# Optimization experiments

Hardware: AMD Instinct MI355X
Metric: run time of the kernel (lower is better)

The kernel has to match this reference:

```python
import jax, jax.numpy as jnp
import numpy as np
from jax.ops import segment_sum

N_NODES = 100000
N_EDGES = 1250000
IN_CH = 64
HID_CH = 64
OUT_CH = 32
NUM_GRAPHS = 128


def setup_inputs() -> dict:
    key = jax.random.key(0)
    ks = jax.random.split(key, 6)
    x = jax.random.normal(ks[0], (N_NODES, IN_CH), dtype=jnp.float32)
    edge_index = jax.random.randint(ks[1], (2, N_EDGES), 0, N_NODES, dtype=jnp.int64)
    batch = jnp.sort(jax.random.randint(ks[2], (N_NODES,), 0, NUM_GRAPHS, dtype=jnp.int64))
    # Glorot-ish scaled weights, zero biases (PyG GCNConv defaults)
    W1 = jax.random.normal(ks[3], (IN_CH, HID_CH), dtype=jnp.float32) * (1.0 / np.sqrt(IN_CH))
    b1 = jnp.zeros((HID_CH,), dtype=jnp.float32)
    W2 = jax.random.normal(ks[4], (HID_CH, OUT_CH), dtype=jnp.float32) * (1.0 / np.sqrt(HID_CH))
    b2 = jnp.zeros((OUT_CH,), dtype=jnp.float32)
    return {"x": x, "edge_index": edge_index, "batch": batch,
            "W1": W1, "b1": b1, "W2": W2, "b2": b2}


def _gcn_conv(x, W, b, src, dst, deg_inv_sqrt):
    # GCNConv: out = D^{-1/2} (A + I) D^{-1/2} (x W) + b
    h = x @ W  # [N, C_out]
    # per-edge normalized messages: gather -> scale -> scatter-add
    msgs = h[src] * (deg_inv_sqrt[src] * deg_inv_sqrt[dst])[:, None]  # [E, C_out]
    agg = segment_sum(msgs, dst, num_segments=N_NODES)
    # self-loop contribution: dinv[i]^2 * h[i]
    agg = agg + h * (deg_inv_sqrt * deg_inv_sqrt)[:, None]
    return agg + b


def reference(x, edge_index, batch, W1, b1, W2, b2):
    src, dst = edge_index[0], edge_index[1]
    # degree with self-loops (GCNConv add_self_loops=True, in-degree of dst)
    ones = jnp.ones((N_EDGES,), dtype=x.dtype)
    deg = segment_sum(ones, dst, num_segments=N_NODES) + 1.0
    deg_inv_sqrt = jax.lax.rsqrt(deg)

    h = _gcn_conv(x, W1, b1, src, dst, deg_inv_sqrt)
    h = jax.nn.relu(h)
    # dropout: eval mode -> identity
    h = _gcn_conv(h, W2, b2, src, dst, deg_inv_sqrt)

    # global mean pool over graphs in the batch
    sums = segment_sum(h, batch, num_segments=NUM_GRAPHS)  # [G, OUT_CH]
    counts = segment_sum(jnp.ones((N_NODES,), dtype=h.dtype), batch, num_segments=NUM_GRAPHS)
    return sums / jnp.maximum(counts, 1.0)[:, None]
```

## Files before the change

kernel.cpp:

```cpp
#include <hip/hip_runtime.h>

#define NN 100000
#define NE 1250000
#define CIN 64
#define CH 64
#define CO 32
#define NG 128
#define NBUCK 98
#define BSHIFT 10
#define EPB 2048
#define NBLKP ((NE + EPB - 1) / EPB)
#define PSLOT 16384
#define CSLOT 24576
#define NTILE (NN / 16)
#define GB ((NTILE + 3) / 4)

typedef unsigned short ushortT;
typedef __attribute__((ext_vector_type(8))) short bfrag;
typedef __attribute__((ext_vector_type(4))) float ffrag;

static __device__ inline ushortT f2bf(float v) {
  unsigned int u = __float_as_uint(v);
  u += 0x7FFFu + ((u >> 16) & 1u);
  return (ushortT)(u >> 16);
}
static __device__ inline float bf2f(ushortT s) {
  return __uint_as_float(((unsigned int)s) << 16);
}
static __device__ inline bfrag pack8(float4 lo, float4 hi) {
  bfrag r;
  r[0] = (short)f2bf(lo.x); r[1] = (short)f2bf(lo.y);
  r[2] = (short)f2bf(lo.z); r[3] = (short)f2bf(lo.w);
  r[4] = (short)f2bf(hi.x); r[5] = (short)f2bf(hi.y);
  r[6] = (short)f2bf(hi.z); r[7] = (short)f2bf(hi.w);
  return r;
}

static __global__ void k_zero(float* __restrict__ sums, int* __restrict__ bcursor,
                              const int* __restrict__ batch, float* __restrict__ counts,
                              const float* __restrict__ W1, ushortT* __restrict__ W1T,
                              const float* __restrict__ W2, ushortT* __restrict__ W2T,
                              ushortT* __restrict__ h) {
  int i = blockIdx.x * 256 + threadIdx.x;
  if (i < NG * CO) sums[i] = 0.0f;
  if (i < 128) bcursor[i] = i * PSLOT;
  if (i < CH) h[(size_t)NN * CH + i] = 0;
  if (i < CIN * CH) W1T[i] = f2bf(W1[(i & 63) * CH + (i >> 6)]);
  if (i < CH * CO) W2T[i] = f2bf(W2[(i & 63) * CO + (i >> 6)]);
  if (blockIdx.x == 0 && threadIdx.x < NG) {
    int g = threadIdx.x;
    int lo = 0, hi = NN;
    while (lo < hi) { int m = (lo + hi) >> 1; if (batch[m] < g) lo = m + 1; else hi = m; }
    int lb = lo;
    lo = 0; hi = NN;
    while (lo < hi) { int m = (lo + hi) >> 1; if (batch[m] <= g) lo = m + 1; else hi = m; }
    counts[g] = (float)(lo - lb);
  }
}

static __global__ __launch_bounds__(256) void k_part(const int* __restrict__ src,
                                                     const int* __restrict__ dst,
                                                     int* __restrict__ bcursor,
                                                     unsigned int* __restrict__ pairs) {
  __shared__ int lh[128], lbase[128], loff[128];
  if (threadIdx.x < 128) { lh[threadIdx.x] = 0; loff[threadIdx.x] = 0; }
  __syncthreads();
  int e0 = blockIdx.x * EPB, e1 = min(e0 + EPB, NE);
  for (int e = e0 + threadIdx.x; e < e1; e += 256)
    atomicAdd(&lh[dst[e] >> BSHIFT], 1);
  __syncthreads();
  if (threadIdx.x < 128) {
    int v = lh[threadIdx.x];
    lbase[threadIdx.x] = v ? atomicAdd(&bcursor[threadIdx.x], v) : 0;
  }
  __syncthreads();
  for (int e = e0 + threadIdx.x; e < e1; e += 256) {
    int d = dst[e], b = d >> BSHIFT;
    int o = atomicAdd(&loff[b], 1);
    pairs[lbase[b] + o] = (unsigned int)src[e] | ((unsigned int)(d & 1023) << 17);
  }
}

static __global__ __launch_bounds__(1024) void k_bucket(const unsigned int* __restrict__ pairs,
                                                        const int* __restrict__ bcursor,
                                                        int* __restrict__ rowstart,
                                                        int* __restrict__ degi,
                                                        float* __restrict__ dinv,
                                                        int* __restrict__ csr_src) {
  __shared__ int lh[1024];
  __shared__ int tmp[1024];
  __shared__ int cur[1024];
  int t = threadIdx.x;
  int b = blockIdx.x, nb = b << BSHIFT;
  lh[t] = 0;
  __syncthreads();
  int p0 = b * PSLOT, p1 = bcursor[b];
  for (int p = p0 + t; p < p1; p += 1024)
    atomicAdd(&lh[pairs[p] >> 17], 1);
  __syncthreads();
  int node = nb + t;
  int raw = lh[t];
  int pd = (raw + 7) & ~7;
  tmp[t] = pd;
  __syncthreads();
  for (int off = 1; off < 1024; off <<= 1) {
    int add = (t >= off) ? tmp[t - off] : 0;
    __syncthreads();
    tmp[t] += add;
    __syncthreads();
  }
  int ex = tmp[t] - pd;
  int rs = b * CSLOT + ex;
  if (node < NN) {
    rowstart[node] = rs;
    degi[node] = pd >> 3;
    dinv[node] = rsqrtf((float)raw + 1.0f);
  }
  cur[t] = rs;
  __syncthreads();
  for (int p = p0 + t; p < p1; p += 1024) {
    unsigned int pk = pairs[p];
    int pos = atomicAdd(&cur[pk >> 17], 1);
    csr_src[pos] = (int)(pk & 0x1FFFFu);
  }
  __syncthreads();
  for (int q = raw; q < pd; ++q) csr_src[rs + q] = NN;
}

static __global__ __launch_bounds__(256) void k_gemm1(const float* __restrict__ x,
                                                      const ushortT* __restrict__ W1T,
                                                      const float* __restrict__ dinv,
                                                      ushortT* __restrict__ h) {
  int wave = threadIdx.x >> 6, lane = threadIdx.x & 63;
  int tile = blockIdx.x * 4 + wave;
  if (tile >= NTILE) return;
  int m = lane & 15;
  int kb = (lane >> 4) * 8;
  int row = tile * 16 + m;
  const float* xr = x + (size_t)row * CIN;
  float4 a0l = *(const float4*)(xr + kb);
  float4 a0h = *(const float4*)(xr + kb + 4);
  float4 a1l = *(const float4*)(xr + kb + 32);
  float4 a1h = *(const float4*)(xr + kb + 36);
  bfrag A0 = pack8(a0l, a0h);
  bfrag A1 = pack8(a1l, a1h);
  int nl = lane & 15;
  ffrag z = {0.f, 0.f, 0.f, 0.f};
  bfrag B00 = *(const bfrag*)(W1T + (0 * 16 + nl) * CIN + kb);
  bfrag B01 = *(const bfrag*)(W1T + (0 * 16 + nl) * CIN + kb + 32);
  bfrag B10 = *(const bfrag*)(W1T + (1 * 16 + nl) * CIN + kb);
  bfrag B11 = *(const bfrag*)(W1T + (1 * 16 + nl) * CIN + kb + 32);
  bfrag B20 = *(const bfrag*)(W1T + (2 * 16 + nl) * CIN + kb);
  bfrag B21 = *(const bfrag*)(W1T + (2 * 16 + nl) * CIN + kb + 32);
  bfrag B30 = *(const bfrag*)(W1T + (3 * 16 + nl) * CIN + kb);
  bfrag B31 = *(const bfrag*)(W1T + (3 * 16 + nl) * CIN + kb + 32);
  ffrag c0 = __builtin_amdgcn_mfma_f32_16x16x32_bf16(A0, B00, z, 0, 0, 0);
  c0 = __builtin_amdgcn_mfma_f32_16x16x32_bf16(A1, B01, c0, 0, 0, 0);
  ffrag c1 = __builtin_amdgcn_mfma_f32_16x16x32_bf16(A0, B10, z, 0, 0, 0);
  c1 = __builtin_amdgcn_mfma_f32_16x16x32_bf16(A1, B11, c1, 0, 0, 0);
  ffrag c2 = __builtin_amdgcn_mfma_f32_16x16x32_bf16(A0, B20, z, 0, 0, 0);
  c2 = __builtin_amdgcn_mfma_f32_16x16x32_bf16(A1, B21, c2, 0, 0, 0);
  ffrag c3 = __builtin_amdgcn_mfma_f32_16x16x32_bf16(A0, B30, z, 0, 0, 0);
  c3 = __builtin_amdgcn_mfma_f32_16x16x32_bf16(A1, B31, c3, 0, 0, 0);
  int rbase = tile * 16 + (lane >> 4) * 4;
  float d0 = dinv[rbase + 0], d1 = dinv[rbase + 1], d2 = dinv[rbase + 2], d3 = dinv[rbase + 3];
  ushortT* hb = h + (size_t)rbase * CH + nl;
  hb[0 * CH + 0]  = f2bf(c0[0] * d0); hb[1 * CH + 0]  = f2bf(c0[1] * d1);
  hb[2 * CH + 0]  = f2bf(c0[2] * d2); hb[3 * CH + 0]  = f2bf(c0[3] * d3);
  hb[0 * CH + 16] = f2bf(c1[0] * d0); hb[1 * CH + 16] = f2bf(c1[1] * d1);
  hb[2 * CH + 16] = f2bf(c1[2] * d2); hb[3 * CH + 16] = f2bf(c1[3] * d3);
  hb[0 * CH + 32] = f2bf(c2[0] * d0); hb[1 * CH + 32] = f2bf(c2[1] * d1);
  hb[2 * CH + 32] = f2bf(c2[2] * d2); hb[3 * CH + 32] = f2bf(c2[3] * d3);
  hb[0 * CH + 48] = f2bf(c3[0] * d0); hb[1 * CH + 48] = f2bf(c3[1] * d1);
  hb[2 * CH + 48] = f2bf(c3[2] * d2); hb[3 * CH + 48] = f2bf(c3[3] * d3);
}

static __global__ __launch_bounds__(256) void k_agg64(const ushortT* __restrict__ h,
                                                      const float* __restrict__ dinv,
                                                      const int* __restrict__ rowstart,
                                                      const int* __restrict__ degi,
                                                      const int* __restrict__ csr_src,
                                                      const float* __restrict__ b1,
                                                      ushortT* __restrict__ aggb) {
  int wave = threadIdx.x >> 6, lane = threadIdx.x & 63;
  int i = __builtin_amdgcn_readfirstlane(blockIdx.x * 4 + wave);
  float bias = b1[lane];
  float acc = bf2f(h[(size_t)i * CH + lane]);
  int s0 = rowstart[i], niter = degi[i];
  for (int it = 0; it < niter; ++it) {
    int base = s0 + it * 8;
    int i0 = csr_src[base + 0];
    int i1 = csr_src[base + 1];
    int i2 = csr_src[base + 2];
    int i3 = csr_src[base + 3];
    int i4 = csr_src[base + 4];
    int i5 = csr_src[base + 5];
    int i6 = csr_src[base + 6];
    int i7 = csr_src[base + 7];
    float a0 = bf2f(h[(size_t)i0 * CH + lane]);
    float a1 = bf2f(h[(size_t)i1 * CH + lane]);
    float a2 = bf2f(h[(size_t)i2 * CH + lane]);
    float a3 = bf2f(h[(size_t)i3 * CH + lane]);
    float a4 = bf2f(h[(size_t)i4 * CH + lane]);
    float a5 = bf2f(h[(size_t)i5 * CH + lane]);
    float a6 = bf2f(h[(size_t)i6 * CH + lane]);
    float a7 = bf2f(h[(size_t)i7 * CH + lane]);
    acc += ((a0 + a1) + (a2 + a3)) + ((a4 + a5) + (a6 + a7));
  }
  float v = acc * dinv[i] + bias;
  aggb[(size_t)i * CH + lane] = f2bf(v > 0.0f ? v : 0.0f);
}

static __global__ __launch_bounds__(256) void k_gemm2(const ushortT* __restrict__ aggb,
                                                      const ushortT* __restrict__ W2T,
                                                      const float* __restrict__ dinv,
                                                      ushortT* __restrict__ h2) {
  if (blockIdx.x == 0 && threadIdx.x < CO) h2[(size_t)NN * CO + threadIdx.x] = 0;
  int wave = threadIdx.x >> 6, lane = threadIdx.x & 63;
  int tile = blockIdx.x * 4 + wave;
  if (tile >= NTILE) return;
  int m = lane & 15;
  int kb = (lane >> 4) * 8;
  int row = tile * 16 + m;
  bfrag A0 = *(const bfrag*)(aggb + (size_t)row * CH + kb);
  bfrag A1 = *(const bfrag*)(aggb + (size_t)row * CH + kb + 32);
  int nl = lane & 15;
  ffrag z = {0.f, 0.f, 0.f, 0.f};
  bfrag B00 = *(const bfrag*)(W2T + (0 * 16 + nl) * CH + kb);
  bfrag B01 = *(const bfrag*)(W2T + (0 * 16 + nl) * CH + kb + 32);
  bfrag B10 = *(const bfrag*)(W2T + (1 * 16 + nl) * CH + kb);
  bfrag B11 = *(const bfrag*)(W2T + (1 * 16 + nl) * CH + kb + 32);
  ffrag c0 = __builtin_amdgcn_mfma_f32_16x16x32_bf16(A0, B00, z, 0, 0, 0);
  c0 = __builtin_amdgcn_mfma_f32_16x16x32_bf16(A1, B01, c0, 0, 0, 0);
  ffrag c1 = __builtin_amdgcn_mfma_f32_16x16x32_bf16(A0, B10, z, 0, 0, 0);
  c1 = __builtin_amdgcn_mfma_f32_16x16x32_bf16(A1, B11, c1, 0, 0, 0);
  int rbase = tile * 16 + (lane >> 4) * 4;
  float d0 = dinv[rbase + 0], d1 = dinv[rbase + 1], d2 = dinv[rbase + 2], d3 = dinv[rbase + 3];
  ushortT* hb = h2 + (size_t)rbase * CO + nl;
  hb[0 * CO + 0]  = f2bf(c0[0] * d0); hb[1 * CO + 0]  = f2bf(c0[1] * d1);
  hb[2 * CO + 0]  = f2bf(c0[2] * d2); hb[3 * CO + 0]  = f2bf(c0[3] * d3);
  hb[0 * CO + 16] = f2bf(c1[0] * d0); hb[1 * CO + 16] = f2bf(c1[1] * d1);
  hb[2 * CO + 16] = f2bf(c1[2] * d2); hb[3 * CO + 16] = f2bf(c1[3] * d3);
}

static __global__ __launch_bounds__(256) void k_agg32pool(const ushortT* __restrict__ h2,
                                                          const float* __restrict__ dinv,
                                                          const int* __restrict__ rowstart,
                                                          const int* __restrict__ degi,
                                                          const int* __restrict__ csr_src,
                                                          const int* __restrict__ batch,
                                                          const float* __restrict__ b2,
                                                          float* __restrict__ sums) {
  __shared__ float vals[4][CO];
  __shared__ int gid[4];
  int wave = threadIdx.x >> 6, lane = threadIdx.x & 63;
  int g = lane >> 5;
  int j = lane & 31;
  int i = __builtin_amdgcn_readfirstlane(blockIdx.x * 4 + wave);
  int s0 = rowstart[i], niter = degi[i];
  float acc = 0.0f;
  for (int it = 0; it < niter; ++it) {
    int base = s0 + it * 8;
    int i0 = csr_src[base + 0];
    int i1 = csr_src[base + 1];
    int i2 = csr_src[base + 2];
    int i3 = csr_src[base + 3];
    int i4 = csr_src[base + 4];
    int i5 = csr_src[base + 5];
    int i6 = csr_src[base + 6];
    int i7 = csr_src[base + 7];
    int sa = g ? i1 : i0;
    int sb = g ? i3 : i2;
    int sc = g ? i5 : i4;
    int sd = g ? i7 : i6;
    float a = bf2f(h2[(size_t)sa * CO + j]);
    float b = bf2f(h2[(size_t)sb * CO + j]);
    float c = bf2f(h2[(size_t)sc * CO + j]);
    float d = bf2f(h2[(size_t)sd * CO + j]);
    acc += (a + b) + (c + d);
  }
  acc += __shfl_xor(acc, 32);
  if (g == 0) {
    acc += bf2f(h2[(size_t)i * CO + j]);
    vals[wave][j] = acc * dinv[i] + b2[j];
    if (j == 0) gid[wave] = batch[i];
  }
  __syncthreads();
  if (threadIdx.x < 32) {
    int ch = threadIdx.x;
    float run = vals[0][ch];
    int gg = gid[0];
    for (int s = 1; s < 4; ++s) {
      if (gid[s] == gg) run += vals[s][ch];
      else { atomicAdd(&sums[gg * CO + ch], run); gg = gid[s]; run = vals[s][ch]; }
    }
    atomicAdd(&sums[gg * CO + ch], run);
  }
}

static __global__ void k_final(const float* __restrict__ sums, const float* __restrict__ counts,
                               float* __restrict__ out) {
  int t = blockIdx.x * 256 + threadIdx.x;
  if (t >= NG * CO) return;
  out[t] = sums[t] / fmaxf(counts[t >> 5], 1.0f);
}

extern "C" void kernel_launch(void* const* d_in, const int* in_sizes, int n_in,
                              void* d_out, int out_size, void* d_ws, size_t ws_size,
                              hipStream_t stream) {
  const float* x   = (const float*)d_in[0];
  const int* ei    = (const int*)d_in[1];
  const int* batch = (const int*)d_in[2];
  const float* W1  = (const float*)d_in[3];
  const float* b1  = (const float*)d_in[4];
  const float* W2  = (const float*)d_in[5];
  const float* b2  = (const float*)d_in[6];
  float* out = (float*)d_out;

  const int* src = ei;
  const int* dst = ei + NE;

  char* base = (char*)d_ws;
  size_t off = 0;
  auto allocB = [&](size_t nbytes) {
    void* p = (void*)(base + off);
    off += ((nbytes + 255) / 256) * 256;
    return p;
  };
  int* degi      = (int*)allocB(NN * 4);
  int* rowstart  = (int*)allocB(NN * 4);
  float* dinv    = (float*)allocB(NN * 4);
  int* bcursor   = (int*)allocB(128 * 4);
  ushortT* W1T   = (ushortT*)allocB(CIN * CH * 2);
  ushortT* W2T   = (ushortT*)allocB(CH * CO * 2);
  int* csr_src   = (int*)allocB((size_t)NBUCK * CSLOT * 4);
  ushortT* hbuf  = (ushortT*)allocB((size_t)(NN + 1) * CH * 2);
  ushortT* aggb  = (ushortT*)allocB((size_t)(NN + 1) * CH * 2);
  float* sums    = (float*)allocB(NG * CO * 4);
  float* counts  = (float*)allocB(NG * 4);
  unsigned int* pairs = (unsigned int*)aggb;

  dim3 B(256);
  k_zero<<<dim3(16), B, 0, stream>>>(sums, bcursor, batch, counts, W1, W1T, W2, W2T, hbuf);
  k_part<<<dim3(NBLKP), B, 0, stream>>>(src, dst, bcursor, pairs);
  k_bucket<<<dim3(NBUCK), dim3(1024), 0, stream>>>(pairs, bcursor, rowstart, degi, dinv, csr_src);
  k_gemm1<<<dim3(GB), B, 0, stream>>>(x, W1T, dinv, hbuf);
  k_agg64<<<dim3(NN / 4), B, 0, stream>>>(hbuf, dinv, rowstart, degi, csr_src, b1, aggb);
  k_gemm2<<<dim3(GB), B, 0, stream>>>(aggb, W2T, dinv, hbuf);
  k_agg32pool<<<dim3(NN / 4), B, 0, stream>>>(hbuf, dinv, rowstart, degi, csr_src, batch, b2, sums);
  k_final<<<dim3(16), B, 0, stream>>>(sums, counts, out);
}
```

Measured before the change: 160.6 us.

## Process four destination nodes per wave in both aggregation kernels

Each wave now aggregates four nodes at once instead of one, interleaving their neighbor gathers in the same loop iteration so more independent loads are in flight. Nodes with fewer neighbor groups clamp their index and are masked with a zero multiplier, which adds redundant loads when degrees differ. The pooling kernel's block reduction now covers 16 nodes, so fewer atomics are issued, and the grid is reduced by four. Register use rises and work is imbalanced within a wave by the maximum degree of its four nodes.

Result: faster. 131.7 us (-18.0%).

```diff
diff --git a/kernel.cpp b/kernel.cpp
--- a/kernel.cpp
+++ b/kernel.cpp
@@ -183,32 +183,51 @@
                                                       const float* __restrict__ b1,
                                                       ushortT* __restrict__ aggb) {
   int wave = threadIdx.x >> 6, lane = threadIdx.x & 63;
-  int i = __builtin_amdgcn_readfirstlane(blockIdx.x * 4 + wave);
+  int i0n = __builtin_amdgcn_readfirstlane(blockIdx.x * 16 + wave * 4);
   float bias = b1[lane];
-  float acc = bf2f(h[(size_t)i * CH + lane]);
-  int s0 = rowstart[i], niter = degi[i];
-  for (int it = 0; it < niter; ++it) {
-    int base = s0 + it * 8;
-    int i0 = csr_src[base + 0];
-    int i1 = csr_src[base + 1];
-    int i2 = csr_src[base + 2];
-    int i3 = csr_src[base + 3];
-    int i4 = csr_src[base + 4];
-    int i5 = csr_src[base + 5];
-    int i6 = csr_src[base + 6];
-    int i7 = csr_src[base + 7];
-    float a0 = bf2f(h[(size_t)i0 * CH + lane]);
-    float a1 = bf2f(h[(size_t)i1 * CH + lane]);
-    float a2 = bf2f(h[(size_t)i2 * CH + lane]);
-    float a3 = bf2f(h[(size_t)i3 * CH + lane]);
-    float a4 = bf2f(h[(size_t)i4 * CH + lane]);
-    float a5 = bf2f(h[(size_t)i5 * CH + lane]);
-    float a6 = bf2f(h[(size_t)i6 * CH + lane]);
-    float a7 = bf2f(h[(size_t)i7 * CH + lane]);
-    acc += ((a0 + a1) + (a2 + a3)) + ((a4 + a5) + (a6 + a7));
-  }
-  float v = acc * dinv[i] + bias;
-  aggb[(size_t)i * CH + lane] = f2bf(v > 0.0f ? v : 0.0f);
+  float acc0 = bf2f(h[(size_t)(i0n + 0) * CH + lane]);
+  float acc1 = bf2f(h[(size_t)(i0n + 1) * CH + lane]);
+  float acc2 = bf2f(h[(size_t)(i0n + 2) * CH + lane]);
+  float acc3 = bf2f(h[(size_t)(i0n + 3) * CH + lane]);
+  int s0 = rowstart[i0n + 0], n0 = degi[i0n + 0];
+  int s1 = rowstart[i0n + 1], n1 = degi[i0n + 1];
+  int s2 = rowstart[i0n + 2], n2 = degi[i0n + 2];
+  int s3 = rowstart[i0n + 3], n3 = degi[i0n + 3];
+  int nmax = max(max(n0, n1), max(n2, n3));
+  for (int it = 0; it < nmax; ++it) {
+    int b0 = s0 + (n0 ? min(it, n0 - 1) : 0) * 8;
+    int b1x = s1 + (n1 ? min(it, n1 - 1) : 0) * 8;
+    int b2 = s2 + (n2 ? min(it, n2 - 1) : 0) * 8;
+    int b3 = s3 + (n3 ? min(it, n3 - 1) : 0) * 8;
+    float m0 = it < n0 ? 1.0f : 0.0f;
+    float m1 = it < n1 ? 1.0f : 0.0f;
+    float m2 = it < n2 ? 1.0f : 0.0f;
+    float m3 = it < n3 ? 1.0f : 0.0f;
+    float t0 = 0.f, t1 = 0.f, t2 = 0.f, t3 = 0.f;
+#pragma unroll
+    for (int q = 0; q < 8; ++q) {
+      int ia = csr_src[b0 + q];
+      int ib = csr_src[b1x + q];
+      int ic = csr_src[b2 + q];
+      int id = csr_src[b3 + q];
+      t0 += bf2f(h[(size_t)ia * CH + lane]);
+      t1 += bf2f(h[(size_t)ib * CH + lane]);
+      t2 += bf2f(h[(size_t)ic * CH + lane]);
+      t3 += bf2f(h[(size_t)id * CH + lane]);
+    }
+    acc0 += m0 * t0;
+    acc1 += m1 * t1;
+    acc2 += m2 * t2;
+    acc3 += m3 * t3;
+  }
+  float v0 = acc0 * dinv[i0n + 0] + bias;
+  float v1 = acc1 * dinv[i0n + 1] + bias;
+  float v2 = acc2 * dinv[i0n + 2] + bias;
+  float v3 = acc3 * dinv[i0n + 3] + bias;
+  aggb[(size_t)(i0n + 0) * CH + lane] = f2bf(v0 > 0.0f ? v0 : 0.0f);
+  aggb[(size_t)(i0n + 1) * CH + lane] = f2bf(v1 > 0.0f ? v1 : 0.0f);
+  aggb[(size_t)(i0n + 2) * CH + lane] = f2bf(v2 > 0.0f ? v2 : 0.0f);
+  aggb[(size_t)(i0n + 3) * CH + lane] = f2bf(v3 > 0.0f ? v3 : 0.0f);
 }
 
 static __global__ __launch_bounds__(256) void k_gemm2(const ushortT* __restrict__ aggb,
@@ -251,46 +270,71 @@
                                                           const int* __restrict__ batch,
                                                           const float* __restrict__ b2,
                                                           float* __restrict__ sums) {
-  __shared__ float vals[4][CO];
-  __shared__ int gid[4];
+  __shared__ float vals[16][CO];
+  __shared__ int gid[16];
   int wave = threadIdx.x >> 6, lane = threadIdx.x & 63;
   int g = lane >> 5;
   int j = lane & 31;
-  int i = __builtin_amdgcn_readfirstlane(blockIdx.x * 4 + wave);
-  int s0 = rowstart[i], niter = degi[i];
-  float acc = 0.0f;
-  for (int it = 0; it < niter; ++it) {
-    int base = s0 + it * 8;
-    int i0 = csr_src[base + 0];
-    int i1 = csr_src[base + 1];
-    int i2 = csr_src[base + 2];
-    int i3 = csr_src[base + 3];
-    int i4 = csr_src[base + 4];
-    int i5 = csr_src[base + 5];
-    int i6 = csr_src[base + 6];
-    int i7 = csr_src[base + 7];
-    int sa = g ? i1 : i0;
-    int sb = g ? i3 : i2;
-    int sc = g ? i5 : i4;
-    int sd = g ? i7 : i6;
-    float a = bf2f(h2[(size_t)sa * CO + j]);
-    float b = bf2f(h2[(size_t)sb * CO + j]);
-    float c = bf2f(h2[(size_t)sc * CO + j]);
-    float d = bf2f(h2[(size_t)sd * CO + j]);
-    acc += (a + b) + (c + d);
-  }
-  acc += __shfl_xor(acc, 32);
+  int i0n = __builtin_amdgcn_readfirstlane(blockIdx.x * 16 + wave * 4);
+  int s0 = rowstart[i0n + 0], n0 = degi[i0n + 0];
+  int s1 = rowstart[i0n + 1], n1 = degi[i0n + 1];
+  int s2 = rowstart[i0n + 2], n2 = degi[i0n + 2];
+  int s3 = rowstart[i0n + 3], n3 = degi[i0n + 3];
+  float acc0 = 0.f, acc1 = 0.f, acc2 = 0.f, acc3 = 0.f;
+  int nmax = max(max(n0, n1), max(n2, n3));
+  for (int it = 0; it < nmax; ++it) {
+    int b0 = s0 + (n0 ? min(it, n0 - 1) : 0) * 8;
+    int b1x = s1 + (n1 ? min(it, n1 - 1) : 0) * 8;
+    int b2 = s2 + (n2 ? min(it, n2 - 1) : 0) * 8;
+    int b3 = s3 + (n3 ? min(it, n3 - 1) : 0) * 8;
+    float m0 = it < n0 ? 1.0f : 0.0f;
+    float m1 = it < n1 ? 1.0f : 0.0f;
+    float m2 = it < n2 ? 1.0f : 0.0f;
+    float m3 = it < n3 ? 1.0f : 0.0f;
+    float t0 = 0.f, t1 = 0.f, t2 = 0.f, t3 = 0.f;
+#pragma unroll
+    for (int q = 0; q < 4; ++q) {
+      int ia = csr_src[b0 + q * 2 + g];
+      int ib = csr_src[b1x + q * 2 + g];
+      int ic = csr_src[b2 + q * 2 + g];
+      int id = csr_src[b3 + q * 2 + g];
+      t0 += bf2f(h2[(size_t)ia * CO + j]);
+      t1 += bf2f(h2[(size_t)ib * CO + j]);
+      t2 += bf2f(h2[(size_t)ic * CO + j]);
+      t3 += bf2f(h2[(size_t)id * CO + j]);
+    }
+    acc0 += m0 * t0;
+    acc1 += m1 * t1;
+    acc2 += m2 * t2;
+    acc3 += m3 * t3;
+  }
+  acc0 += __shfl_xor(acc0, 32);
+  acc1 += __shfl_xor(acc1, 32);
+  acc2 += __shfl_xor(acc2, 32);
+  acc3 += __shfl_xor(acc3, 32);
   if (g == 0) {
-    acc += bf2f(h2[(size_t)i * CO + j]);
-    vals[wave][j] = acc * dinv[i] + b2[j];
-    if (j == 0) gid[wave] = batch[i];
+    acc0 += bf2f(h2[(size_t)(i0n + 0) * CO + j]);
+    acc1 += bf2f(h2[(size_t)(i0n + 1) * CO + j]);
+    acc2 += bf2f(h2[(size_t)(i0n + 2) * CO + j]);
+    acc3 += bf2f(h2[(size_t)(i0n + 3) * CO + j]);
+    float bb = b2[j];
+    vals[wave * 4 + 0][j] = acc0 * dinv[i0n + 0] + bb;
+    vals[wave * 4 + 1][j] = acc1 * dinv[i0n + 1] + bb;
+    vals[wave * 4 + 2][j] = acc2 * dinv[i0n + 2] + bb;
+    vals[wave * 4 + 3][j] = acc3 * dinv[i0n + 3] + bb;
+    if (j == 0) {
+      gid[wave * 4 + 0] = batch[i0n + 0];
+      gid[wave * 4 + 1] = batch[i0n + 1];
+      gid[wave * 4 + 2] = batch[i0n + 2];
+      gid[wave * 4 + 3] = batch[i0n + 3];
+    }
   }
   __syncthreads();
   if (threadIdx.x < 32) {
     int ch = threadIdx.x;
     float run = vals[0][ch];
     int gg = gid[0];
-    for (int s = 1; s < 4; ++s) {
+    for (int s = 1; s < 16; ++s) {
       if (gid[s] == gg) run += vals[s][ch];
       else { atomicAdd(&sums[gg * CO + ch], run); gg = gid[s]; run = vals[s][ch]; }
     }
@@ -345,8 +389,8 @@
   k_part<<<dim3(NBLKP), B, 0, stream>>>(src, dst, bcursor, pairs);
   k_bucket<<<dim3(NBUCK), dim3(1024), 0, stream>>>(pairs, bcursor, rowstart, degi, dinv, csr_src);
   k_gemm1<<<dim3(GB), B, 0, stream>>>(x, W1T, dinv, hbuf);
-  k_agg64<<<dim3(NN / 4), B, 0, stream>>>(hbuf, dinv, rowstart, degi, csr_src, b1, aggb);
+  k_agg64<<<dim3(NN / 16), B, 0, stream>>>(hbuf, dinv, rowstart, degi, csr_src, b1, aggb);
   k_gemm2<<<dim3(GB), B, 0, stream>>>(aggb, W2T, dinv, hbuf);
-  k_agg32pool<<<dim3(NN / 4), B, 0, stream>>>(hbuf, dinv, rowstart, degi, csr_src, batch, b2, sums);
+  k_agg32pool<<<dim3(NN / 16), B, 0, stream>>>(hbuf, dinv, rowstart, degi, csr_src, batch, b2, sums);
   k_final<<<dim3(16), B, 0, stream>>>(sums, counts, out);
 }
```
